# Kernel tuning notes

Hardware: AMD Instinct MI355X
Metric: run time of the kernel (lower is better)

## Reference

```python
import jax, jax.numpy as jnp
import numpy as np
from jax import lax

L, B, T = 512, 1024, 48


def setup_inputs() -> dict:
    key = jax.random.key(0)
    k1, k2, k3, k4, k5 = jax.random.split(key, 5)
    emissions = jax.random.normal(k1, (L, B, T), dtype=jnp.float32)
    tags = jax.random.randint(k2, (L, B), 0, T)
    mask = jnp.ones((L, B), dtype=bool)
    start_transitions = jax.random.uniform(k3, (T,), minval=-0.1, maxval=0.1, dtype=jnp.float32)
    end_transitions = jax.random.uniform(k4, (T,), minval=-0.1, maxval=0.1, dtype=jnp.float32)
    transitions = jax.random.uniform(k5, (T, T), minval=-0.1, maxval=0.1, dtype=jnp.float32)
    return {
        'emissions': emissions,
        'tags': tags,
        'mask': mask,
        'start_transitions': start_transitions,
        'end_transitions': end_transitions,
        'transitions': transitions,
    }


def reference(emissions, tags, mask, start_transitions, end_transitions, transitions):
    # emissions: [L, B, T] float; tags: [L, B] int; mask: [L, B] bool (seq-first)
    fm = mask.astype(emissions.dtype)
    seq_len, batch, _ = emissions.shape
    b_idx = jnp.arange(batch)

    # ---- numerator: score of the gold path ----
    # emission score at each step: emissions[i, b, tags[i, b]] -> [L, B]
    em_sc = jnp.take_along_axis(emissions, tags[:, :, None], axis=2)[:, :, 0]
    # transition score between consecutive tags -> [L-1, B]
    trans_sc = transitions[tags[:-1], tags[1:]]
    score = start_transitions[tags[0]] + em_sc[0]
    score = score + jnp.sum((trans_sc + em_sc[1:]) * fm[1:], axis=0)
    seq_ends = mask.astype(jnp.int32).sum(axis=0) - 1  # [B]
    last_tags = tags[seq_ends, b_idx]
    score = score + end_transitions[last_tags]

    # ---- denominator: log partition via forward algorithm (scan) ----
    alpha0 = start_transitions + emissions[0]  # [B, T]

    def step(alpha, xs):
        em, m = xs  # em: [B, T], m: [B]
        # [B, T(prev), T(next)] logsumexp over prev
        next_alpha = jax.nn.logsumexp(
            alpha[:, :, None] + transitions[None, :, :] + em[:, None, :], axis=1)
        alpha = jnp.where(m[:, None], next_alpha, alpha)
        return alpha, None

    alpha, _ = lax.scan(step, alpha0, (emissions[1:], mask[1:]))
    denominator = jax.nn.logsumexp(alpha + end_transitions, axis=1)  # [B]

    llh = score - denominator
    return jnp.mean(llh)  # reduction='mean' (default)
```

## Files before the change

kernel.cpp:

```cpp
#include <hip/hip_runtime.h>

#define LSEQ 512
#define BATCH 1024
#define T 48
#define CHUNK 8
#define NCH (LSEQ / CHUNK)

static __device__ __forceinline__ float bcast_lane0(float x) {
    return __int_as_float(__builtin_amdgcn_readfirstlane(__float_as_int(x)));
}
static __device__ __forceinline__ float rl(float x, int i) {
    return __int_as_float(__builtin_amdgcn_readlane(__float_as_int(x), i));
}
static __device__ __forceinline__ float fast_rcp(float x) {
#if __has_builtin(__builtin_amdgcn_rcpf)
    return __builtin_amdgcn_rcpf(x);
#else
    return 1.0f / x;
#endif
}

#define PIN4(a,b,c,d) asm volatile("" : "+v"(a), "+v"(b), "+v"(c), "+v"(d))
#define PIN_E(E) do { \
    PIN4(E[ 0],E[ 1],E[ 2],E[ 3]); PIN4(E[ 4],E[ 5],E[ 6],E[ 7]); \
    PIN4(E[ 8],E[ 9],E[10],E[11]); PIN4(E[12],E[13],E[14],E[15]); \
    PIN4(E[16],E[17],E[18],E[19]); PIN4(E[20],E[21],E[22],E[23]); \
    PIN4(E[24],E[25],E[26],E[27]); PIN4(E[28],E[29],E[30],E[31]); \
    PIN4(E[32],E[33],E[34],E[35]); PIN4(E[36],E[37],E[38],E[39]); \
    PIN4(E[40],E[41],E[42],E[43]); PIN4(E[44],E[45],E[46],E[47]); \
} while (0)

static __device__ __forceinline__ void crf_step(
    float& w, float& C, float em, int mk, bool valid, const float* E)
{
    const float em0 = bcast_lane0(em);
    const float e   = __expf(em - em0);
    float s0 = 0.f, s1 = 0.f, s2 = 0.f, s3 = 0.f;
    #pragma unroll
    for (int i = 0; i < T; i += 4) {
        s0 = __builtin_fmaf(rl(w, i + 0), E[i + 0], s0);
        s1 = __builtin_fmaf(rl(w, i + 1), E[i + 1], s1);
        s2 = __builtin_fmaf(rl(w, i + 2), E[i + 2], s2);
        s3 = __builtin_fmaf(rl(w, i + 3), E[i + 3], s3);
    }
    const float S    = (s0 + s1) + (s2 + s3);
    const float S0   = bcast_lane0(S);
    const float rs   = fast_rcp(S0);
    const float lg   = __logf(S0);
    const float wnew = (e * rs) * S;
    const bool  upd  = (mk != 0);
    w = (upd && valid) ? wnew : w;
    C = upd ? (C + em0 + lg) : C;
}

__global__ __launch_bounds__(256, 1) void crf_forward(
    const float* __restrict__ emissions,
    const int* __restrict__ mask,
    const float* __restrict__ start_tr,
    const float* __restrict__ end_tr,
    const float* __restrict__ trans,
    float* __restrict__ denom_out)
{
    const int tid  = threadIdx.x;
    const int wave = tid >> 6, lane = tid & 63;
    const int b    = blockIdx.x * 4 + wave;
    const bool valid = (lane < T);
    const int jc   = valid ? lane : (T - 1);

    float E[T];
    #pragma unroll
    for (int i = 0; i < T; ++i) E[i] = __expf(trans[i * T + jc]);

    const float* emb = emissions + (size_t)b * T + jc;
    const int*   mkb = mask + b;

    const float a0 = start_tr[jc] + emb[0];
    const float A0 = bcast_lane0(a0);
    float w = valid ? __expf(a0 - A0) : 0.f;
    float C = A0;

    float emA[CHUNK], emB[CHUNK];
    int   mkA[CHUNK], mkB[CHUNK];
    #pragma unroll
    for (int u = 0; u < CHUNK; ++u) {
        const int tt = 1 + u;
        emA[u] = emb[(size_t)tt * (BATCH * T)];
        mkA[u] = mkb[tt * BATCH];
    }

    for (int c = 0; c < NCH; c += 2) {
        PIN_E(E);
        {
            const int tB = 1 + (c + 1) * CHUNK;
            #pragma unroll
            for (int u = 0; u < CHUNK; ++u) {
                const int tt = tB + u;
                const bool ok = (tt <= LSEQ - 1);
                const int tc = ok ? tt : (LSEQ - 1);
                emB[u] = emb[(size_t)tc * (BATCH * T)];
                mkB[u] = ok ? mkb[tc * BATCH] : 0;
            }
        }
        {
            #pragma unroll
            for (int u = 0; u < CHUNK; ++u)
                crf_step(w, C, emA[u], mkA[u], valid, E);
        }
        {
            const int tA = 1 + (c + 2) * CHUNK;
            #pragma unroll
            for (int u = 0; u < CHUNK; ++u) {
                const int tt = tA + u;
                const bool ok = (tt <= LSEQ - 1);
                const int tc = ok ? tt : (LSEQ - 1);
                emA[u] = emb[(size_t)tc * (BATCH * T)];
                mkA[u] = ok ? mkb[tc * BATCH] : 0;
            }
        }
        {
            #pragma unroll
            for (int u = 0; u < CHUNK; ++u)
                crf_step(w, C, emB[u], mkB[u], valid, E);
        }
    }

    float v = valid ? (w * __expf(end_tr[jc])) : 0.f;
    #pragma unroll
    for (int off = 32; off > 0; off >>= 1) v += __shfl_xor(v, off);
    if (lane == 0) denom_out[b] = C + __logf(v);
}

__global__ __launch_bounds__(256) void crf_score_partial(
    const float* __restrict__ emissions,
    const int* __restrict__ tags,
    const int* __restrict__ mask,
    const float* __restrict__ trans,
    float* __restrict__ part,
    int* __restrict__ cnt,
    int csz)
{
    const int gid = blockIdx.x * blockDim.x + threadIdx.x;
    const int b = gid & (BATCH - 1);
    const int c = gid >> 10;
    const int t0 = c * csz;
    const int t1 = t0 + csz;

    float sc = 0.f;
    int ct = 0;
    const int tstart = (t0 == 0) ? 1 : t0;
    if (t0 == 0) ct += mask[b] ? 1 : 0;

    int tag_prev = tags[(tstart - 1) * BATCH + b];
    for (int t = tstart; t < t1; ++t) {
        const int tag = tags[t * BATCH + b];
        const int mt = mask[t * BATCH + b];
        if (mt) {
            sc += trans[tag_prev * T + tag]
                + emissions[((size_t)t * BATCH + b) * T + tag];
            ct += 1;
        }
        tag_prev = tag;
    }
    part[gid] = sc;
    cnt[gid] = ct;
}

__global__ __launch_bounds__(1024) void crf_combine(
    const float* __restrict__ emissions,
    const int* __restrict__ tags,
    const float* __restrict__ start_tr,
    const float* __restrict__ end_tr,
    const float* __restrict__ part,
    const int* __restrict__ cnt,
    const float* __restrict__ denom,
    float* __restrict__ out,
    int nchunk)
{
    const int b = threadIdx.x;

    const int tag0 = tags[b];
    float sc = start_tr[tag0] + emissions[(size_t)b * T + tag0];
    int ct = 0;
    for (int c = 0; c < nchunk; ++c) {
        sc += part[c * BATCH + b];
        ct += cnt[c * BATCH + b];
    }
    if (ct < 1) ct = 1;
    const int last_tag = tags[(ct - 1) * BATCH + b];
    sc += end_tr[last_tag];

    const float llh = sc - denom[b];

    __shared__ float red[1024];
    red[b] = llh;
    __syncthreads();
    #pragma unroll
    for (int s = 512; s > 0; s >>= 1) {
        if (b < s) red[b] += red[b + s];
        __syncthreads();
    }
    if (b == 0) out[0] = red[0] / (float)BATCH;
}

extern "C" void kernel_launch(void* const* d_in, const int* in_sizes, int n_in,
                              void* d_out, int out_size, void* d_ws, size_t ws_size,
                              hipStream_t stream) {
    const float* emissions        = (const float*)d_in[0];
    const int* tags               = (const int*)d_in[1];
    const int* mask               = (const int*)d_in[2];
    const float* start_tr         = (const float*)d_in[3];
    const float* end_tr           = (const float*)d_in[4];
    const float* trans            = (const float*)d_in[5];
    float* out                    = (float*)d_out;

    const int nchunk = (ws_size >= (size_t)(BATCH * 4 + 32 * BATCH * 8 + 64)) ? 32 : 8;
    const int csz    = LSEQ / nchunk;

    float* denom = (float*)d_ws;
    float* part  = denom + BATCH;
    int*   cnt   = (int*)(part + nchunk * BATCH);

    crf_forward<<<256, 256, 0, stream>>>(emissions, mask, start_tr, end_tr, trans, denom);
    crf_score_partial<<<nchunk * BATCH / 256, 256, 0, stream>>>(
        emissions, tags, mask, trans, part, cnt, csz);
    crf_combine<<<1, 1024, 0, stream>>>(emissions, tags, start_tr, end_tr,
                                        part, cnt, denom, out, nchunk);
}
```

Before: 218.5 us.

## Broadcast forward-algorithm state through LDS instead of per-lane readlane

```diff
diff --git a/kernel.cpp b/kernel.cpp
--- a/kernel.cpp
+++ b/kernel.cpp
@@ -8,9 +8,6 @@
 
 static __device__ __forceinline__ float bcast_lane0(float x) {
     return __int_as_float(__builtin_amdgcn_readfirstlane(__float_as_int(x)));
-}
-static __device__ __forceinline__ float rl(float x, int i) {
-    return __int_as_float(__builtin_amdgcn_readlane(__float_as_int(x), i));
 }
 static __device__ __forceinline__ float fast_rcp(float x) {
 #if __has_builtin(__builtin_amdgcn_rcpf)
@@ -31,26 +28,33 @@
 } while (0)
 
 static __device__ __forceinline__ void crf_step(
-    float& w, float& C, float em, int mk, bool valid, const float* E)
+    float W[T], float& w_self, float& C, float em, int mk,
+    const float E[T], float* __restrict__ lds, int lane)
 {
     const float em0 = bcast_lane0(em);
     const float e   = __expf(em - em0);
     float s0 = 0.f, s1 = 0.f, s2 = 0.f, s3 = 0.f;
     #pragma unroll
     for (int i = 0; i < T; i += 4) {
-        s0 = __builtin_fmaf(rl(w, i + 0), E[i + 0], s0);
-        s1 = __builtin_fmaf(rl(w, i + 1), E[i + 1], s1);
-        s2 = __builtin_fmaf(rl(w, i + 2), E[i + 2], s2);
-        s3 = __builtin_fmaf(rl(w, i + 3), E[i + 3], s3);
+        s0 = __builtin_fmaf(W[i + 0], E[i + 0], s0);
+        s1 = __builtin_fmaf(W[i + 1], E[i + 1], s1);
+        s2 = __builtin_fmaf(W[i + 2], E[i + 2], s2);
+        s3 = __builtin_fmaf(W[i + 3], E[i + 3], s3);
     }
     const float S    = (s0 + s1) + (s2 + s3);
-    const float S0   = bcast_lane0(S);
-    const float rs   = fast_rcp(S0);
-    const float lg   = __logf(S0);
-    const float wnew = (e * rs) * S;
+    const float rs   = fast_rcp(W[0]);
+    const float lg   = __logf(W[0]);
+    const float unew = (e * rs) * S;
     const bool  upd  = (mk != 0);
-    w = (upd && valid) ? wnew : w;
-    C = upd ? (C + em0 + lg) : C;
+    w_self = upd ? unew : w_self;
+    C      = upd ? (C + em0 + lg) : C;
+    lds[lane] = w_self;
+    #pragma unroll
+    for (int k = 0; k < T / 4; ++k) {
+        const float4 v = ((const float4*)lds)[k];
+        W[4 * k + 0] = v.x; W[4 * k + 1] = v.y;
+        W[4 * k + 2] = v.z; W[4 * k + 3] = v.w;
+    }
 }
 
 __global__ __launch_bounds__(256, 1) void crf_forward(
@@ -61,23 +65,34 @@
     const float* __restrict__ trans,
     float* __restrict__ denom_out)
 {
+    __shared__ float Wlds[4][64];
     const int tid  = threadIdx.x;
     const int wave = tid >> 6, lane = tid & 63;
     const int b    = blockIdx.x * 4 + wave;
     const bool valid = (lane < T);
     const int jc   = valid ? lane : (T - 1);
+    float* lds = &Wlds[wave][0];
 
     float E[T];
     #pragma unroll
     for (int i = 0; i < T; ++i) E[i] = __expf(trans[i * T + jc]);
+    PIN_E(E);
 
     const float* emb = emissions + (size_t)b * T + jc;
     const int*   mkb = mask + b;
 
     const float a0 = start_tr[jc] + emb[0];
     const float A0 = bcast_lane0(a0);
-    float w = valid ? __expf(a0 - A0) : 0.f;
+    float w_self = __expf(a0 - A0);
     float C = A0;
+    lds[lane] = w_self;
+    float W[T];
+    #pragma unroll
+    for (int k = 0; k < T / 4; ++k) {
+        const float4 v = ((const float4*)lds)[k];
+        W[4 * k + 0] = v.x; W[4 * k + 1] = v.y;
+        W[4 * k + 2] = v.z; W[4 * k + 3] = v.w;
+    }
 
     float emA[CHUNK], emB[CHUNK];
     int   mkA[CHUNK], mkB[CHUNK];
@@ -89,7 +104,6 @@
     }
 
     for (int c = 0; c < NCH; c += 2) {
-        PIN_E(E);
         {
             const int tB = 1 + (c + 1) * CHUNK;
             #pragma unroll
@@ -101,11 +115,9 @@
                 mkB[u] = ok ? mkb[tc * BATCH] : 0;
             }
         }
-        {
-            #pragma unroll
-            for (int u = 0; u < CHUNK; ++u)
-                crf_step(w, C, emA[u], mkA[u], valid, E);
-        }
+        #pragma unroll
+        for (int u = 0; u < CHUNK; ++u)
+            crf_step(W, w_self, C, emA[u], mkA[u], E, lds, lane);
         {
             const int tA = 1 + (c + 2) * CHUNK;
             #pragma unroll
@@ -117,14 +129,12 @@
                 mkA[u] = ok ? mkb[tc * BATCH] : 0;
             }
         }
-        {
-            #pragma unroll
-            for (int u = 0; u < CHUNK; ++u)
-                crf_step(w, C, emB[u], mkB[u], valid, E);
-        }
-    }
-
-    float v = valid ? (w * __expf(end_tr[jc])) : 0.f;
+        #pragma unroll
+        for (int u = 0; u < CHUNK; ++u)
+            crf_step(W, w_self, C, emB[u], mkB[u], E, lds, lane);
+    }
+
+    float v = valid ? (w_self * __expf(end_tr[jc])) : 0.f;
     #pragma unroll
     for (int off = 32; off > 0; off >>= 1) v += __shfl_xor(v, off);
     if (lane == 0) denom_out[b] = C + __logf(v);
```

Result: slower. 300.5 us (+37.6%).
